# Optimization experiments

Hardware: AMD Instinct MI355X
Metric: run time of the kernel (lower is better)

Reference implementation:

```python
import jax, jax.numpy as jnp
import numpy as np

B, N, D_IN, D_OUT = 8, 2048, 1024, 1024

def setup_inputs() -> dict:
    key = jax.random.key(0)
    kx, kq, kk, kv = jax.random.split(key, 4)
    scale = 1.0 / np.sqrt(D_IN)
    return {
        "x": jax.random.normal(kx, (B, N, D_IN), dtype=jnp.float32),
        "Wq": jax.random.normal(kq, (D_IN, D_OUT), dtype=jnp.float32) * scale,
        "Wk": jax.random.normal(kk, (D_IN, D_OUT), dtype=jnp.float32) * scale,
        "Wv": jax.random.normal(kv, (D_IN, D_OUT), dtype=jnp.float32) * scale,
    }

def reference(x, Wq, Wk, Wv):
    # Projections (qkv_bias=False)
    q = x @ Wq  # [B, N, d_out]
    k = x @ Wk
    v = x @ Wv
    n = x.shape[1]
    scores = jnp.einsum('bqd,bkd->bqk', q, k)  # [B, N, N]
    causal_mask = jnp.triu(jnp.ones((n, n), dtype=bool), k=1)
    scores = jnp.where(causal_mask, -jnp.inf, scores)
    inv_sqrt_d = jnp.asarray(1.0 / np.sqrt(q.shape[-1]), dtype=scores.dtype)
    attn = jax.nn.softmax(scores * inv_sqrt_d, axis=-1)
    # dropout p=0.0 -> identity
    return jnp.einsum('bqk,bkd->bqd', attn, v)
```

## Files before the change

kernel.cpp:

```cpp
#include <hip/hip_runtime.h>
#include <hip/hip_bf16.h>

#define DI __device__ __forceinline__

typedef __bf16 bf16x8 __attribute__((ext_vector_type(8)));
typedef float  f32x4  __attribute__((ext_vector_type(4)));
typedef unsigned int u32x4 __attribute__((ext_vector_type(4)));

DI unsigned short f2bf(float f) {
    unsigned int u = __float_as_uint(f);
    u += 0x7fffu + ((u >> 16) & 1u);
    return (unsigned short)(u >> 16);
}

DI unsigned cvtpk_bf16(float lo, float hi) {
    unsigned r;
    asm("v_cvt_pk_bf16_f32 %0, %1, %2" : "=v"(r) : "v"(lo), "v"(hi));
    return r;
}

DI void gload16(const unsigned short* g, unsigned short* l) {
    __builtin_amdgcn_global_load_lds(
        (const __attribute__((address_space(1))) unsigned int*)g,
        (__attribute__((address_space(3))) unsigned int*)l, 16, 0, 0);
}

__global__ void convert_x(const float* __restrict__ x, unsigned short* __restrict__ Xb) {
    int i = blockIdx.x * 256 + threadIdx.x;
    float4 v = reinterpret_cast<const float4*>(x)[i];
    ushort4 o;
    o.x = f2bf(v.x); o.y = f2bf(v.y); o.z = f2bf(v.z); o.w = f2bf(v.w);
    reinterpret_cast<ushort4*>(Xb)[i] = o;
}

__global__ void convert_w(const float* __restrict__ Wq, const float* __restrict__ Wk,
                          const float* __restrict__ Wv, unsigned short* __restrict__ Wt) {
    __shared__ float t[32][33];
    const int z = blockIdx.z;
    const float* W = (z == 0) ? Wq : (z == 1 ? Wk : Wv);
    const float scale = (z == 0) ? 0.03125f : 1.0f;
    const int n0 = blockIdx.x * 32, k0 = blockIdx.y * 32;
    const int tx = threadIdx.x, ty = threadIdx.y;
#pragma unroll
    for (int i = 0; i < 4; ++i)
        t[ty + i * 8][tx] = W[(size_t)(k0 + ty + i * 8) * 1024 + n0 + tx];
    __syncthreads();
#pragma unroll
    for (int i = 0; i < 4; ++i)
        Wt[(size_t)(z * 1024 + n0 + ty + i * 8) * 1024 + k0 + tx] =
            f2bf(t[tx][ty + i * 8] * scale);
}

#define BAR    asm volatile("s_barrier" ::: "memory")
#define WAITV4 asm volatile("s_waitcnt vmcnt(4)" ::: "memory")
#define WAITV3 asm volatile("s_waitcnt vmcnt(3)" ::: "memory")
#define WAITV0 asm volatile("s_waitcnt vmcnt(0)" ::: "memory")


#define READ_A(SLOT, MH)                                                      \
    _Pragma("unroll")                                                         \
    for (int fi = 0; fi < 4; ++fi)                                            \
        _Pragma("unroll")                                                     \
        for (int kk = 0; kk < 2; ++kk)                                        \
            aR[fi][kk] = *reinterpret_cast<const bf16x8*>(                    \
                lsA + (SLOT) * 16384 + (MH) * 8192 +                          \
                ((abase ^ (kk * 32)) + fi * 1024));

#define READ_B(SLOT, NH, BS)                                                  \
    _Pragma("unroll")                                                         \
    for (int fj = 0; fj < 2; ++fj)                                            \
        _Pragma("unroll")                                                     \
        for (int kk = 0; kk < 2; ++kk)                                        \
            BS[fj][kk] = *reinterpret_cast<const bf16x8*>(                    \
                lsB + (SLOT) * 16384 + (NH) * 8192 +                          \
                ((bbase ^ (kk * 32)) + fj * 1024));

#define STAGE_A(KT, H)                                                        \
    {                                                                         \
        unsigned uA_ = (unsigned)(m0 + (H) * 128) * 1024u + (unsigned)(KT) * 64u; \
        _Pragma("unroll")                                                     \
        for (int it = 0; it < 2; ++it)                                        \
            gload16(Ab + uA_ + sAoff[it],                                     \
                    lsA + (((KT) & 1) * 2 + (H)) * 8192 + it * 4096 + tid * 8);\
    }

#define STAGE_B(KT, H)                                                        \
    {                                                                         \
        unsigned uB_ = (unsigned)(n0 + (H) * 128) * 1024u + (unsigned)(KT) * 64u; \
        _Pragma("unroll")                                                     \
        for (int it = 0; it < 2; ++it)                                        \
            gload16(Bb + uB_ + sBoff[it],                                     \
                    lsB + (((KT) & 1) * 2 + (H)) * 8192 + it * 4096 + tid * 8);\
    }

#define MMA_PHASE(MH, NH, BS)                                                 \
    __builtin_amdgcn_s_setprio(1);                                            \
    _Pragma("unroll")                                                         \
    for (int kk = 0; kk < 2; ++kk)                                            \
        _Pragma("unroll")                                                     \
        for (int fi = 0; fi < 4; ++fi)                                        \
            _Pragma("unroll")                                                 \
            for (int fj = 0; fj < 2; ++fj)                                    \
                acc[(MH) * 4 + fi][(NH) * 2 + fj] =                           \
                    __builtin_amdgcn_mfma_f32_16x16x32_bf16(                  \
                        aR[fi][kk], BS[fj][kk],                               \
                        acc[(MH) * 4 + fi][(NH) * 2 + fj], 0, 0, 0);          \
    __builtin_amdgcn_s_setprio(0);

__global__ __launch_bounds__(512) void gemm256(
    const unsigned short* __restrict__ A0, const unsigned short* __restrict__ B0,
    unsigned short* __restrict__ Oq, unsigned short* __restrict__ Ok,
    unsigned short* __restrict__ Ov)
{
    extern __shared__ char smem_raw[];
    unsigned short* lsA = (unsigned short*)smem_raw;
    unsigned short* lsB = lsA + 32768;

    const int tid = threadIdx.x;
    const int lane = tid & 63;
    const int wid = tid >> 6;
    const int wm = wid >> 2, wn = wid & 3;
    const int lr = lane & 15, lg = lane >> 4;

    const int m0 = blockIdx.x * 256, n0 = blockIdx.y * 256;
    const int NT = 16;
    const unsigned short* Ab = A0;
    const unsigned short* Bb = B0;

    const unsigned chm = (unsigned)(lg ^ (lr & 7));
    const unsigned abase = (unsigned)(wm * 64 + lr) * 64u + chm * 8u;
    const unsigned bbase = (unsigned)(wn * 32 + lr) * 64u + chm * 8u;
    unsigned sAoff[2], sBoff[2];
#pragma unroll
    for (int it = 0; it < 2; ++it) {
        const unsigned idx = it * 512 + tid;
        const unsigned row = idx >> 3;
        const unsigned ch = (idx & 7) ^ (row & 7);
        sAoff[it] = row * 1024u + ch * 8u;
        sBoff[it] = row * 1024u + ch * 8u;
    }

    f32x4 acc[8][4] = {};
    bf16x8 aR[4][2], b0[2][2], b1[2][2];

    STAGE_A(0, 0); STAGE_A(0, 1); STAGE_B(0, 0); STAGE_B(0, 1);
    STAGE_A(1, 0); STAGE_B(1, 0);
    WAITV4; BAR;

    for (int kt = 0; kt < NT; ++kt) {
        const int slot = kt & 1;
        const bool s1 = (kt + 1) < NT, s2 = (kt + 2) < NT;
        READ_A(slot, 0); READ_B(slot, 0, b0);
        if (s1) { STAGE_A(kt + 1, 1); }
        BAR; MMA_PHASE(0, 0, b0);
        READ_B(slot, 1, b1);
        if (s1) { STAGE_B(kt + 1, 1); }
        BAR; MMA_PHASE(0, 1, b1);
        READ_A(slot, 1);
        if (s2) { STAGE_A(kt + 2, 0); }
        BAR; MMA_PHASE(1, 0, b0);
        if (s2) {
            STAGE_B(kt + 2, 0);
            WAITV4;
        } else {
            WAITV0;
        }
        BAR; MMA_PHASE(1, 1, b1);
    }

#pragma unroll
    for (int i = 0; i < 8; ++i) {
        const int rl = (i >> 2) * 128 + wm * 64 + (i & 3) * 16 + lg * 4;
#pragma unroll
        for (int j = 0; j < 4; ++j) {
            const int cl = (j >> 1) * 128 + wn * 32 + (j & 1) * 16 + lr;
            f32x4 v = acc[i][j];
            const int gm = m0 + rl;
            const int z = n0 >> 10;
            const int cin = (n0 & 1023) + cl;
            if (z == 2) {
                const int b = gm >> 11, nib = gm & 2047;
                ushort4 h;
                h.x = f2bf(v[0]); h.y = f2bf(v[1]); h.z = f2bf(v[2]); h.w = f2bf(v[3]);
                *reinterpret_cast<ushort4*>(
                    &Ov[(size_t)b * 2097152u + (size_t)cin * 2048 + nib]) = h;
            } else {
                unsigned short* O = z ? Ok : Oq;
#pragma unroll
                for (int r2 = 0; r2 < 4; ++r2)
                    O[(size_t)(gm + r2) * 1024 + cin] = f2bf(v[r2]);
            }
        }
    }
}

template <int MODE>
__global__ __launch_bounds__(512, 4) void gemm_attn(
    const unsigned short* __restrict__ A0, const unsigned short* __restrict__ B0,
    void* __restrict__ Cf0)
{
    __shared__ alignas(16) unsigned short lds[3 * 12288];

    const int tid = threadIdx.x;
    const int lane = tid & 63;
    const int wid = tid >> 6;
    const int wm = wid >> 2, wn = wid & 3;
    const int lr = lane & 15, lg = lane >> 4;

    int r128, n0, NT, bz;
    constexpr unsigned STRB = (MODE == 2) ? 2048u : 1024u;

    if constexpr (MODE == 1) {
        const int idx = blockIdx.x;
        bz = idx & 7;
        r128 = (idx >> 3) & 15;
        const int c256 = idx >> 7;
        if (c256 > (r128 >> 1)) return;
        n0 = c256 * 256; NT = 32;
    } else {
        const int idx = blockIdx.x;
        const int k5 = idx >> 5;
        r128 = (k5 < 8) ? (15 - k5) : (k5 - 8);
        const int nt4 = (idx >> 3) & 3;
        bz = idx & 7;
        n0 = nt4 * 256; NT = 4 * (r128 + 1);
    }
    const int r256 = r128 >> 1;
    const unsigned short* Bb = B0 + (size_t)bz * 2097152u;

    const unsigned short* Ab;
    size_t cbase;
    if constexpr (MODE == 1) {
        Ab = A0 + (size_t)bz * 2097152u;
        cbase = ((size_t)bz * 36 + (size_t)(r256 * (r256 + 1) / 2) + (n0 >> 8)) * 65536u +
                (size_t)(r128 & 1) * 32768u;
    } else {
        Ab = A0 + ((size_t)bz * 36 + (size_t)(r256 * (r256 + 1) / 2)) * 65536u;
        cbase = (size_t)bz * 2097152u + (size_t)(r128 * 128) * 1024u;
    }

    const unsigned fswl = (unsigned)((lr ^ (lr >> 2)) & 3);
    const unsigned abase = (unsigned)(wm * 64 + lr) * 32u + ((unsigned)lg ^ fswl) * 8u;
    const unsigned bbase = 4096u + (unsigned)(wn * 32 + lr) * 32u + ((unsigned)lg ^ fswl) * 8u;

    const unsigned rowA = (unsigned)(tid >> 2);
    const unsigned chA = ((unsigned)tid & 3u) ^ (unsigned)((rowA ^ (rowA >> 2)) & 3u);
    unsigned sAoff;
    if constexpr (MODE == 1)
        sAoff = ((unsigned)(r128 * 128) + rowA) * 1024u + chA * 8u;
    else
        sAoff = ((unsigned)((r128 & 1) * 128) + rowA) * 256u + chA * 8u;
    unsigned sBoff[2];
#pragma unroll
    for (int it = 0; it < 2; ++it) {
        const unsigned idx = it * 512 + tid;
        const unsigned rowB = idx >> 2;
        const unsigned chB = (idx & 3u) ^ (unsigned)((rowB ^ (rowB >> 2)) & 3u);
        sBoff[it] = ((unsigned)n0 + rowB) * STRB + chB * 8u;
    }

#define AT_STAGE(KT, SL)                                                      \
    {                                                                         \
        unsigned u_;                                                          \
        if constexpr (MODE == 2)                                              \
            u_ = ((unsigned)((KT) >> 3)) * 65536u + ((KT) & 7) * 32u;         \
        else                                                                  \
            u_ = (unsigned)(KT) * 32u;                                        \
        gload16(Ab + u_ + sAoff, lds + (SL) * 12288 + tid * 8);               \
        gload16(Bb + (unsigned)(KT) * 32u + sBoff[0],                         \
                lds + (SL) * 12288 + 4096 + tid * 8);                         \
        gload16(Bb + (unsigned)(KT) * 32u + sBoff[1],                         \
                lds + (SL) * 12288 + 8192 + tid * 8);                         \
    }

    f32x4 acc[4][4] = {};
    bf16x8 aR[4], bv[2];
    float den4[4] = {0.f, 0.f, 0.f, 0.f};
    const int rqb = r128 * 128 + wm * 64 + lr;

    AT_STAGE(0, 0); AT_STAGE(1, 1);

    int sl = 0, st2 = 2;
    for (int kt = 0; kt < NT; ++kt) {
        if (kt + 1 < NT) { WAITV3; } else { WAITV0; }
        BAR;
        if (kt + 2 < NT) { AT_STAGE(kt + 2, st2); }
        const unsigned short* sp = lds + sl * 12288;
#pragma unroll
        for (int fi = 0; fi < 4; ++fi)
            aR[fi] = *reinterpret_cast<const bf16x8*>(sp + abase + fi * 512);
#pragma unroll
        for (int fj = 0; fj < 2; ++fj)
            bv[fj] = *reinterpret_cast<const bf16x8*>(sp + bbase + fj * 512);

        if constexpr (MODE == 2) {
            const bool domask = (kt >= NT - 4);
            const int kbase = kt * 32 + lg * 8;
#pragma unroll
            for (int fi = 0; fi < 4; ++fi) {
                u32x4 su = __builtin_bit_cast(u32x4, aR[fi]);
                float p[8];
#pragma unroll
                for (int c = 0; c < 4; ++c) {
                    p[2 * c]     = __expf(__uint_as_float(su[c] << 16));
                    p[2 * c + 1] = __expf(__uint_as_float(su[c] & 0xffff0000u));
                }
                if (domask) {
                    const int thr = (rqb + fi * 16) - kbase;
#pragma unroll
                    for (int e = 0; e < 8; ++e)
                        p[e] = (e <= thr) ? p[e] : 0.f;
                }
                den4[fi] += ((p[0] + p[1]) + (p[2] + p[3])) +
                            ((p[4] + p[5]) + (p[6] + p[7]));
                u32x4 pk;
#pragma unroll
                for (int c = 0; c < 4; ++c)
                    pk[c] = cvtpk_bf16(p[2 * c], p[2 * c + 1]);
                aR[fi] = __builtin_bit_cast(bf16x8, pk);
            }
        }

        __builtin_amdgcn_s_setprio(1);
#pragma unroll
        for (int fi = 0; fi < 4; ++fi)
#pragma unroll
            for (int fj = 0; fj < 2; ++fj)
                acc[fi][fj] = __builtin_amdgcn_mfma_f32_16x16x32_bf16(
                    aR[fi], bv[fj], acc[fi][fj], 0, 0, 0);
        __builtin_amdgcn_s_setprio(0);
#pragma unroll
        for (int fj = 0; fj < 2; ++fj)
            bv[fj] = *reinterpret_cast<const bf16x8*>(sp + bbase + 4096 + fj * 512);
        __builtin_amdgcn_s_setprio(1);
#pragma unroll
        for (int fi = 0; fi < 4; ++fi)
#pragma unroll
            for (int fj = 0; fj < 2; ++fj)
                acc[fi][2 + fj] = __builtin_amdgcn_mfma_f32_16x16x32_bf16(
                    aR[fi], bv[fj], acc[fi][2 + fj], 0, 0, 0);
        __builtin_amdgcn_s_setprio(0);
        sl = (sl == 2) ? 0 : sl + 1;
        st2 = (st2 == 2) ? 0 : st2 + 1;
    }

    float rinv[4][4];
    if constexpr (MODE == 2) {
#pragma unroll
        for (int fi = 0; fi < 4; ++fi) {
            den4[fi] += __shfl_xor(den4[fi], 16);
            den4[fi] += __shfl_xor(den4[fi], 32);
        }
#pragma unroll
        for (int fi = 0; fi < 4; ++fi)
#pragma unroll
            for (int r2 = 0; r2 < 4; ++r2)
                rinv[fi][r2] = 1.0f / __shfl(den4[fi], lg * 4 + r2);
    }

#pragma unroll
    for (int fi = 0; fi < 4; ++fi) {
        const int rloc = wm * 64 + fi * 16 + lg * 4;
#pragma unroll
        for (int j = 0; j < 4; ++j) {
            const int cloc = (j >> 1) * 128 + wn * 32 + (j & 1) * 16 + lr;
            f32x4 v = acc[fi][j];
            if constexpr (MODE == 1) {
                unsigned short* Cs = (unsigned short*)Cf0;
#pragma unroll
                for (int r2 = 0; r2 < 4; ++r2)
                    Cs[cbase + (size_t)(rloc + r2) * 256 + cloc] = f2bf(v[r2]);
            } else {
                float* Cf = (float*)Cf0;
#pragma unroll
                for (int r2 = 0; r2 < 4; ++r2)
                    Cf[cbase + (size_t)(rloc + r2) * 1024 + (n0 + cloc)] =
                        v[r2] * rinv[fi][r2];
            }
        }
    }
#undef AT_STAGE
}

extern "C" void kernel_launch(void* const* d_in, const int* in_sizes, int n_in,
                              void* d_out, int out_size, void* d_ws, size_t ws_size,
                              hipStream_t stream) {
    const float* x  = (const float*)d_in[0];
    const float* Wq = (const float*)d_in[1];
    const float* Wk = (const float*)d_in[2];
    const float* Wv = (const float*)d_in[3];
    float* out = (float*)d_out;

    char* base = (char*)d_ws;
    unsigned short* Qb = (unsigned short*)(base);
    unsigned short* Kb = (unsigned short*)(base + 33554432u);
    unsigned short* Vt = (unsigned short*)(base + 67108864u);
    unsigned short* Xb = (unsigned short*)(base + 100663296u);
    unsigned short* Wt = (unsigned short*)(base + 134217728u);
    unsigned short* Sb = (unsigned short*)(base + 100663296u);

    hipFuncSetAttribute(reinterpret_cast<const void*>(&gemm256),
                        hipFuncAttributeMaxDynamicSharedMemorySize, 131072);

    convert_x<<<16384, 256, 0, stream>>>(x, Xb);
    convert_w<<<dim3(32, 32, 3), dim3(32, 8), 0, stream>>>(Wq, Wk, Wv, Wt);
    gemm256<<<dim3(64, 12), 512, 131072, stream>>>(Xb, Wt, Qb, Kb, Vt);
    gemm_attn<1><<<1024, 512, 0, stream>>>(Qb, Kb, Sb);
    gemm_attn<2><<<512, 512, 0, stream>>>(Sb, Vt, out);
}
```

Before: 268.8 us.

## Move exp and causal mask into score epilogue; compute row sums via MFMA

The exponentiation and causal masking of scores move out of the PV kernel's inner loop and into the epilogue of the score kernel, which now stores exp(scores) as bf16 with masked entries zeroed. The softmax denominator is no longer built from per-lane sums and shuffles. It comes from an extra MFMA against a vector of ones, so it is computed from the same bf16-rounded probabilities that feed the PV product. This takes VALU exp/convert work off the PV main loop, at the cost of extra MFMA issue per k-step and a heavier epilogue in the score kernel.

```diff
diff --git a/kernel.cpp b/kernel.cpp
--- a/kernel.cpp
+++ b/kernel.cpp
@@ -5,18 +5,11 @@
 
 typedef __bf16 bf16x8 __attribute__((ext_vector_type(8)));
 typedef float  f32x4  __attribute__((ext_vector_type(4)));
-typedef unsigned int u32x4 __attribute__((ext_vector_type(4)));
 
 DI unsigned short f2bf(float f) {
     unsigned int u = __float_as_uint(f);
     u += 0x7fffu + ((u >> 16) & 1u);
     return (unsigned short)(u >> 16);
-}
-
-DI unsigned cvtpk_bf16(float lo, float hi) {
-    unsigned r;
-    asm("v_cvt_pk_bf16_f32 %0, %1, %2" : "=v"(r) : "v"(lo), "v"(hi));
-    return r;
 }
 
 DI void gload16(const unsigned short* g, unsigned short* l) {
@@ -274,9 +267,11 @@
     }
 
     f32x4 acc[4][4] = {};
+    f32x4 accd[4] = {};
     bf16x8 aR[4], bv[2];
-    float den4[4] = {0.f, 0.f, 0.f, 0.f};
-    const int rqb = r128 * 128 + wm * 64 + lr;
+    bf16x8 ones;
+#pragma unroll
+    for (int i = 0; i < 8; ++i) ones[i] = (__bf16)1.0f;
 
     AT_STAGE(0, 0); AT_STAGE(1, 1);
 
@@ -292,35 +287,6 @@
 #pragma unroll
         for (int fj = 0; fj < 2; ++fj)
             bv[fj] = *reinterpret_cast<const bf16x8*>(sp + bbase + fj * 512);
-
-        if constexpr (MODE == 2) {
-            const bool domask = (kt >= NT - 4);
-            const int kbase = kt * 32 + lg * 8;
-#pragma unroll
-            for (int fi = 0; fi < 4; ++fi) {
-                u32x4 su = __builtin_bit_cast(u32x4, aR[fi]);
-                float p[8];
-#pragma unroll
-                for (int c = 0; c < 4; ++c) {
-                    p[2 * c]     = __expf(__uint_as_float(su[c] << 16));
-                    p[2 * c + 1] = __expf(__uint_as_float(su[c] & 0xffff0000u));
-                }
-                if (domask) {
-                    const int thr = (rqb + fi * 16) - kbase;
-#pragma unroll
-                    for (int e = 0; e < 8; ++e)
-                        p[e] = (e <= thr) ? p[e] : 0.f;
-                }
-                den4[fi] += ((p[0] + p[1]) + (p[2] + p[3])) +
-                            ((p[4] + p[5]) + (p[6] + p[7]));
-                u32x4 pk;
-#pragma unroll
-                for (int c = 0; c < 4; ++c)
-                    pk[c] = cvtpk_bf16(p[2 * c], p[2 * c + 1]);
-                aR[fi] = __builtin_bit_cast(bf16x8, pk);
-            }
-        }
-
         __builtin_amdgcn_s_setprio(1);
 #pragma unroll
         for (int fi = 0; fi < 4; ++fi)
@@ -334,28 +300,27 @@
             bv[fj] = *reinterpret_cast<const bf16x8*>(sp + bbase + 4096 + fj * 512);
         __builtin_amdgcn_s_setprio(1);
 #pragma unroll
-        for (int fi = 0; fi < 4; ++fi)
+        for (int fi = 0; fi < 4; ++fi) {
 #pragma unroll
             for (int fj = 0; fj < 2; ++fj)
                 acc[fi][2 + fj] = __builtin_amdgcn_mfma_f32_16x16x32_bf16(
                     aR[fi], bv[fj], acc[fi][2 + fj], 0, 0, 0);
+            if constexpr (MODE == 2)
+                accd[fi] = __builtin_amdgcn_mfma_f32_16x16x32_bf16(
+                    aR[fi], ones, accd[fi], 0, 0, 0);
+        }
         __builtin_amdgcn_s_setprio(0);
         sl = (sl == 2) ? 0 : sl + 1;
         st2 = (st2 == 2) ? 0 : st2 + 1;
     }
 
-    float rinv[4][4];
+    f32x4 rv[4];
     if constexpr (MODE == 2) {
 #pragma unroll
-        for (int fi = 0; fi < 4; ++fi) {
-            den4[fi] += __shfl_xor(den4[fi], 16);
-            den4[fi] += __shfl_xor(den4[fi], 32);
-        }
-#pragma unroll
         for (int fi = 0; fi < 4; ++fi)
 #pragma unroll
             for (int r2 = 0; r2 < 4; ++r2)
-                rinv[fi][r2] = 1.0f / __shfl(den4[fi], lg * 4 + r2);
+                rv[fi][r2] = 1.0f / accd[fi][r2];
     }
 
 #pragma unroll
@@ -367,15 +332,21 @@
             f32x4 v = acc[fi][j];
             if constexpr (MODE == 1) {
                 unsigned short* Cs = (unsigned short*)Cf0;
-#pragma unroll
-                for (int r2 = 0; r2 < 4; ++r2)
-                    Cs[cbase + (size_t)(rloc + r2) * 256 + cloc] = f2bf(v[r2]);
+                const bool diag = ((n0 >> 8) == r256);
+                const int growb = r128 * 128 + rloc;
+                const int gcol = n0 + cloc;
+#pragma unroll
+                for (int r2 = 0; r2 < 4; ++r2) {
+                    float e = __expf(v[r2]);
+                    if (diag && gcol > growb + r2) e = 0.0f;
+                    Cs[cbase + (size_t)(rloc + r2) * 256 + cloc] = f2bf(e);
+                }
             } else {
                 float* Cf = (float*)Cf0;
 #pragma unroll
                 for (int r2 = 0; r2 < 4; ++r2)
                     Cf[cbase + (size_t)(rloc + r2) * 1024 + (n0 + cloc)] =
-                        v[r2] * rinv[fi][r2];
+                        v[r2] * rv[fi][r2];
             }
         }
     }
```

Result: faster. 225.0 us (-16.3%).
